# Optimization experiments

Hardware: AMD Instinct MI355X
Metric: run time of the kernel (lower is better)

Reference implementation:

```python
import jax, jax.numpy as jnp
import numpy as np

L, B, E, H = 512, 32, 1024, 16
NEG = -1e9  # finite stand-in for masked_fill(-inf); avoids NaNs if a row were fully masked


def setup_inputs() -> dict:
    key = jax.random.key(0)
    ks = jax.random.split(key, 6)
    s_in = (2.0 / (3 * E + E)) ** 0.5   # xavier-ish scale for in_proj
    s_out = (2.0 / (E + E)) ** 0.5
    return {
        "query": jax.random.normal(ks[0], (L, B, E), jnp.float32),
        "key": jax.random.normal(ks[1], (L, B, E), jnp.float32),
        "value": jax.random.normal(ks[2], (L, B, E), jnp.float32),
        "attn_mask": jax.random.randint(ks[3], (B, L, L), 0, 2).astype(jnp.bool_),
        "in_proj_weight": jax.random.normal(ks[4], (3 * E, E), jnp.float32) * s_in,
        "in_proj_bias": jnp.zeros((3 * E,), jnp.float32),
        "out_proj_weight": jax.random.normal(ks[5], (E, E), jnp.float32) * s_out,
        "out_proj_bias": jnp.zeros((E,), jnp.float32),
        "num_heads": H,
    }


def reference(query, key, value, attn_mask, in_proj_weight, in_proj_bias,
              out_proj_weight, out_proj_bias, num_heads):
    Lq, Bz, Em = query.shape
    hd = Em // num_heads
    Wq, Wk, Wv = jnp.split(in_proj_weight, 3, axis=0)
    bq, bk, bv = jnp.split(in_proj_bias, 3, axis=0)
    # in-projection: x @ W^T + b  (torch F.linear convention)
    q = query @ Wq.T + bq
    k = key @ Wk.T + bk
    v = value @ Wv.T + bv
    # [L, B, E] -> [B*H, L, hd], batch-major (b*H + h) per torch view semantics
    def split_heads(x):
        return x.reshape(x.shape[0], Bz * num_heads, hd).transpose(1, 0, 2)
    q, k, v = split_heads(q), split_heads(k), split_heads(v)
    q = q / jnp.sqrt(jnp.asarray(hd, q.dtype))
    # scores: [B*H, Lq, Lk]
    attn = jnp.einsum('bqd,bkd->bqk', q, k)
    # mask broadcast to heads: [B, L, L] -> [B*H, L, L] with index b*H + h
    mask_mh = jnp.repeat(attn_mask, num_heads, axis=0)
    # original: scatter zeros where masked, then masked_fill(-inf) inside
    # multi_head_positional_attention; net effect = mask -> -inf before softmax
    attn = jnp.where(mask_mh, NEG, attn)
    p = jax.nn.softmax(attn, axis=-1)
    out = jnp.einsum('bqk,bkd->bqd', p, v)        # [B*H, Lq, hd]
    out = out.transpose(1, 0, 2).reshape(Lq, Bz, Em)
    out = out @ out_proj_weight.T + out_proj_bias  # [L, B, E]
    return out
```

## Files before the change

kernel.cpp:

```cpp
#include <hip/hip_runtime.h>
#include <hip/hip_bf16.h>
#include <stdint.h>

#define LSEQ 512
#define BATCH 32
#define EMB 1024
#define NHEAD 16
#define HDIM 64
#define TOK (LSEQ*BATCH)
#define BHTOT (BATCH*NHEAD)

typedef __attribute__((ext_vector_type(8))) short short8;
typedef __attribute__((ext_vector_type(4))) short short4v;
typedef __attribute__((ext_vector_type(4))) float f32x4;

__device__ __forceinline__ short f2bf(float f) {
  __hip_bfloat16 h = __float2bfloat16(f);
  union { __hip_bfloat16 h; short s; } u; u.h = h;
  return u.s;
}

#if defined(__has_builtin)
#if __has_builtin(__builtin_amdgcn_global_load_lds)
#define HAVE_GLL 1
#endif
#endif

__device__ __forceinline__ void gload_lds16(const void* g, void* l) {
#ifdef HAVE_GLL
  __builtin_amdgcn_global_load_lds((const __attribute__((address_space(1))) void*)g,
                                   (__attribute__((address_space(3))) void*)l, 16, 0, 0);
#else
  *(short8*)l = *(const short8*)g;
#endif
}

#define WAIT_VM8  do { asm volatile("s_waitcnt vmcnt(8)" ::: "memory"); __builtin_amdgcn_sched_barrier(0); } while (0)
#define WAIT_VM4  do { asm volatile("s_waitcnt vmcnt(4)" ::: "memory"); __builtin_amdgcn_sched_barrier(0); } while (0)
#define WAIT_VM0  do { asm volatile("s_waitcnt vmcnt(0)" ::: "memory"); __builtin_amdgcn_sched_barrier(0); } while (0)
#define WAIT_LGKM0 do { asm volatile("s_waitcnt lgkmcnt(0)" ::: "memory"); __builtin_amdgcn_sched_barrier(0); } while (0)
#define BAR() __builtin_amdgcn_s_barrier()

__global__ void castx_kernel(const float* __restrict__ xq, const float* __restrict__ xk,
                             const float* __restrict__ xv, short* __restrict__ xb)
{
  const int stride = 4096 * 256;
  int base = blockIdx.x * 256 + threadIdx.x;
  #pragma unroll
  for (int it = 0; it < 12; ++it) {
    int i = base + it * stride;
    const float* src = (i < 4194304) ? xq : (i < 8388608) ? xk : xv;
    int j = i & 4194303;
    f32x4 v = ((const f32x4*)src)[j];
    short4v o;
    o[0] = f2bf(v[0]); o[1] = f2bf(v[1]); o[2] = f2bf(v[2]); o[3] = f2bf(v[3]);
    ((short4v*)xb)[i] = o;
  }
}

__global__ void cast_weights(const float* __restrict__ W, const float* __restrict__ Wo,
                             const float* __restrict__ bias,
                             short* __restrict__ Wb, short* __restrict__ Wob,
                             float* __restrict__ biasp)
{
  int i = blockIdx.x * 256 + threadIdx.x;
  if (i < 786432) {
    f32x4 v = ((const f32x4*)W)[i];
    int row = i >> 8;
    float s = (row < 1024) ? 0.125f : 1.0f;
    short4v o;
    o[0] = f2bf(v[0]*s); o[1] = f2bf(v[1]*s); o[2] = f2bf(v[2]*s); o[3] = f2bf(v[3]*s);
    ((short4v*)Wb)[i] = o;
  } else {
    int j = i - 786432;
    f32x4 v = ((const f32x4*)Wo)[j];
    short4v o;
    o[0] = f2bf(v[0]); o[1] = f2bf(v[1]); o[2] = f2bf(v[2]); o[3] = f2bf(v[3]);
    ((short4v*)Wob)[j] = o;
  }
  if (i < 768) {
    f32x4 v = ((const f32x4*)bias)[i];
    float s = (i < 256) ? 0.125f : 1.0f;
    f32x4 o = {v[0]*s, v[1]*s, v[2]*s, v[3]*s};
    ((f32x4*)biasp)[i] = o;
  }
}

__global__ void maskbits_kernel(const int* __restrict__ mask, uint32_t* __restrict__ mb)
{
  int w = (blockIdx.x * 256 + threadIdx.x) >> 6;
  int lane = threadIdx.x & 63;
  const int* src = mask + ((size_t)w << 9);
  uint32_t* dst = mb + w * 16;
  #pragma unroll
  for (int c = 0; c < 8; ++c) {
    int v = src[c * 64 + lane];
    unsigned long long m = __ballot(v != 0);
    if (lane == 0) dst[c*2]     = (uint32_t)m;
    if (lane == 1) dst[c*2 + 1] = (uint32_t)(m >> 32);
  }
}


#define FRAG_READ(AsX, BsX)                                           \
    short8 af[4], bfr[4];                                             \
    _Pragma("unroll")                                                 \
    for (int mi = 0; mi < 4; ++mi) {                                  \
      int row = wm + mi * 16 + l15;                                   \
      int cs = l4 ^ ((row >> 1) & 3);                                 \
      af[mi] = *(const short8*)&AsX[row * 32 + cs * 8];               \
    }                                                                 \
    _Pragma("unroll")                                                 \
    for (int ni = 0; ni < 4; ++ni) {                                  \
      int row = wn + ni * 16 + l15;                                   \
      int cs = l4 ^ ((row >> 1) & 3);                                 \
      bfr[ni] = *(const short8*)&BsX[row * 32 + cs * 8];              \
    }

#define DO_MFMA()                                                     \
    _Pragma("unroll")                                                 \
    for (int mi = 0; mi < 4; ++mi)                                    \
      _Pragma("unroll")                                               \
      for (int ni = 0; ni < 4; ++ni)                                  \
        acc[mi][ni] = __builtin_amdgcn_mfma_f32_16x16x32_bf16(af[mi], bfr[ni], acc[mi][ni], 0, 0, 0)

#define ISSUE(AsX, BsX, koff)                                         \
    _Pragma("unroll")                                                 \
    for (int jj = 0; jj < 2; ++jj) {                                  \
      gload_lds16(aSrc[jj] + (koff), &AsX[sDst[jj]]);                 \
      gload_lds16(bSrc[jj] + (koff), &BsX[sDst[jj]]);                 \
    }

#define GSTEP_I(AsX, BsX, WAITM, koff)                                \
  { WAITM; BAR();                                                     \
    FRAG_READ(AsX, BsX);                                              \
    WAIT_LGKM0; BAR();                                                \
    ISSUE(AsX, BsX, koff);                                            \
    DO_MFMA(); }

#define GSTEP_N(AsX, BsX, WAITM)                                      \
  { WAITM; BAR();                                                     \
    FRAG_READ(AsX, BsX);                                              \
    WAIT_LGKM0; BAR();                                                \
    DO_MFMA(); }

#define STAGE_COORDS(Abase, Bbase)                                    \
  const short* aSrc[2]; const short* bSrc[2]; int sDst[2];            \
  _Pragma("unroll")                                                   \
  for (int jj = 0; jj < 2; ++jj) {                                    \
    int ch = tid + jj * 256;                                          \
    int row = ch >> 2, cl = ch & 3;                                   \
    int cs = cl ^ ((row >> 1) & 3);                                   \
    aSrc[jj] = (Abase) + (size_t)(m0 + row) * 1024 + cs * 8;          \
    bSrc[jj] = (Bbase) + (size_t)(n0 + row) * 1024 + cs * 8;          \
    sDst[jj] = ch * 8;                                                \
  }

#define PIPE_BODY()                                                   \
        \
  ISSUE(As0, Bs0, 0); ISSUE(As1, Bs1, 32); ISSUE(As2, Bs2, 64);       \
                \
  for (int i = 0; i < 9; ++i) {                                       \
    const int s = 3 * i;                                              \
    GSTEP_I(As0, Bs0, WAIT_VM8, (s + 3) * 32);                        \
    GSTEP_I(As1, Bs1, WAIT_VM8, (s + 4) * 32);                        \
    GSTEP_I(As2, Bs2, WAIT_VM8, (s + 5) * 32);                        \
  }                                                                   \
           \
  GSTEP_I(As0, Bs0, WAIT_VM8, 30 * 32);                               \
  GSTEP_I(As1, Bs1, WAIT_VM8, 31 * 32);                               \
  GSTEP_N(As2, Bs2, WAIT_VM8);                                        \
  GSTEP_N(As0, Bs0, WAIT_VM4);                                        \
  GSTEP_N(As1, Bs1, WAIT_VM0);

__launch_bounds__(256, 3)
__global__ void proj_gemm(const short* __restrict__ xb, const short* __restrict__ W,
                          const float* __restrict__ biasp,
                          short* __restrict__ qh, short* __restrict__ kh,
                          short* __restrict__ vh)
{
  int z = blockIdx.z;
  const short* A = xb + (size_t)z * TOK * EMB;
  short* C       = (z == 0) ? qh : (z == 1) ? kh : vh;
  const short* B = W + (size_t)z * 1024 * 1024;
  const float* bp = biasp + z * 1024;

  int flat = blockIdx.y * 8 + blockIdx.x;
  int X = flat & 7, s0 = flat >> 3;
  int m0 = (X * 16 + (s0 >> 3)) * 128;
  int n0 = (s0 & 7) * 128;

  __shared__ alignas(16) short As0[128 * 32];
  __shared__ alignas(16) short As1[128 * 32];
  __shared__ alignas(16) short As2[128 * 32];
  __shared__ alignas(16) short Bs0[128 * 32];
  __shared__ alignas(16) short Bs1[128 * 32];
  __shared__ alignas(16) short Bs2[128 * 32];

  const int tid = threadIdx.x, lane = tid & 63;
  const int w = tid >> 6;
  const int wm = (w >> 1) * 64, wn = (w & 1) * 64;
  const int l15 = lane & 15, l4 = lane >> 4;

  STAGE_COORDS(A, B);

  f32x4 acc[4][4];
  #pragma unroll
  for (int mi = 0; mi < 4; ++mi)
    #pragma unroll
    for (int ni = 0; ni < 4; ++ni) acc[mi][ni] = f32x4{0.f, 0.f, 0.f, 0.f};

  PIPE_BODY();

  #pragma unroll
  for (int ni = 0; ni < 4; ++ni) {
    int gcol = n0 + wn + ni * 16 + l15;
    float bv = bp[gcol];
    int h = gcol >> 6, d = gcol & 63;
    #pragma unroll
    for (int mi = 0; mi < 4; ++mi) {
      int growb = m0 + wm + mi * 16 + l4 * 4;
      #pragma unroll
      for (int r = 0; r < 4; ++r) {
        int grow = growb + r;
        int lsq = grow >> 5, bb = grow & 31;
        C[((size_t)((bb * NHEAD + h) * LSEQ + lsq)) * HDIM + d] = f2bf(acc[mi][ni][r] + bv);
      }
    }
  }
}

__launch_bounds__(256, 3)
__global__ void out_gemm(const short* __restrict__ Ab, const short* __restrict__ W,
                         const float* __restrict__ bo, float* __restrict__ out)
{
  int flat = blockIdx.y * 8 + blockIdx.x;
  int X = flat & 7, s0 = flat >> 3;
  int m0 = (X * 16 + (s0 >> 3)) * 128;
  int n0 = (s0 & 7) * 128;

  __shared__ alignas(16) short As0[128 * 32];
  __shared__ alignas(16) short As1[128 * 32];
  __shared__ alignas(16) short As2[128 * 32];
  __shared__ alignas(16) short Bs0[128 * 32];
  __shared__ alignas(16) short Bs1[128 * 32];
  __shared__ alignas(16) short Bs2[128 * 32];

  const int tid = threadIdx.x, lane = tid & 63;
  const int w = tid >> 6;
  const int wm = (w >> 1) * 64, wn = (w & 1) * 64;
  const int l15 = lane & 15, l4 = lane >> 4;

  STAGE_COORDS(Ab, W);

  f32x4 acc[4][4];
  #pragma unroll
  for (int mi = 0; mi < 4; ++mi)
    #pragma unroll
    for (int ni = 0; ni < 4; ++ni) acc[mi][ni] = f32x4{0.f, 0.f, 0.f, 0.f};

  PIPE_BODY();

  #pragma unroll
  for (int ni = 0; ni < 4; ++ni) {
    int gcol = n0 + wn + ni * 16 + l15;
    float bv = bo[gcol];
    #pragma unroll
    for (int mi = 0; mi < 4; ++mi) {
      int growb = m0 + wm + mi * 16 + l4 * 4;
      #pragma unroll
      for (int r = 0; r < 4; ++r)
        out[(size_t)(growb + r) * 1024 + gcol] = acc[mi][ni][r] + bv;
    }
  }
}

__launch_bounds__(256, 2)
__global__ void attn_kernel(const short* __restrict__ qh, const short* __restrict__ kh,
                            const short* __restrict__ vh, const uint32_t* __restrict__ mb,
                            short* __restrict__ ao)
{
  int flat = blockIdx.y * 8 + blockIdx.x;
  int X = flat & 7, s = flat >> 3;
  int bh = X * 64 + (s >> 3);
  int qblk = s & 7;
  int b = bh >> 4, h = bh & 15;
  int q0 = qblk * 64;

  const int tid = threadIdx.x, lane = tid & 63, w = tid >> 6;
  const int l15 = lane & 15, l4 = lane >> 4;

  __shared__ alignas(16) short Ks[64 * 64];
  __shared__ alignas(16) short Vt[64 * 72];
  __shared__ alignas(16) short Ps[4 * 16 * 72];
  __shared__ uint32_t Mw[64 * 2];

  const size_t bhoff = (size_t)bh * (LSEQ * HDIM);

  short8 aq[2];
  {
    int qrow = q0 + w * 16 + l15;
    const short* qp = qh + bhoff + (size_t)qrow * HDIM + l4 * 8;
    aq[0] = *(const short8*)qp;
    aq[1] = *(const short8*)(qp + 32);
  }

  f32x4 oacc[4];
  #pragma unroll
  for (int n = 0; n < 4; ++n) oacc[n] = f32x4{0.f, 0.f, 0.f, 0.f};
  float m_i[4], l_i[4];
  #pragma unroll
  for (int r = 0; r < 4; ++r) { m_i[r] = -1e30f; l_i[r] = 0.f; }

  for (int kt = 0; kt < 8; ++kt) {
    __syncthreads();
    #pragma unroll
    for (int jj = 0; jj < 2; ++jj) {
      int ch = tid + jj * 256;
      int row = ch >> 3, cl = ch & 7;
      int cg = cl ^ (row & 7);
      const short* g = kh + bhoff + (size_t)(kt * 64 + row) * HDIM + cg * 8;
      gload_lds16(g, &Ks[ch * 8]);
    }
    #pragma unroll
    for (int jj = 0; jj < 2; ++jj) {
      int c = tid + jj * 256;
      int kv = c & 63, d0 = (c >> 6) * 8;
      const short* g = vh + bhoff + (size_t)(kt * 64 + kv) * HDIM + d0;
      short8 vv = *(const short8*)g;
      #pragma unroll
      for (int j = 0; j < 8; ++j) Vt[(d0 + j) * 72 + kv] = vv[j];
    }
    if (tid < 128) {
      int qr = tid >> 1, wd = tid & 1;
      Mw[qr * 2 + wd] = mb[((size_t)b * LSEQ + q0 + qr) * 16 + kt * 2 + wd];
    }
    __syncthreads();

    f32x4 sa[4];
    #pragma unroll
    for (int n = 0; n < 4; ++n) sa[n] = f32x4{0.f, 0.f, 0.f, 0.f};
    #pragma unroll
    for (int ss = 0; ss < 2; ++ss) {
      #pragma unroll
      for (int n = 0; n < 4; ++n) {
        int row = n * 16 + l15;
        int cs = (ss * 4 + l4) ^ (row & 7);
        short8 bk = *(const short8*)&Ks[row * 64 + cs * 8];
        sa[n] = __builtin_amdgcn_mfma_f32_16x16x32_bf16(aq[ss], bk, sa[n], 0, 0, 0);
      }
    }

    #pragma unroll
    for (int r = 0; r < 4; ++r) {
      int qr = w * 16 + l4 * 4 + r;
      uint32_t mlo = Mw[qr * 2], mhi = Mw[qr * 2 + 1];
      float sv[4];
      #pragma unroll
      for (int n = 0; n < 4; ++n) {
        int cc = n * 16 + l15;
        uint32_t bit = ((cc < 32 ? (mlo >> cc) : (mhi >> (cc - 32))) & 1u);
        sv[n] = bit ? -1e9f : sa[n][r];
      }
      float rmax = fmaxf(fmaxf(sv[0], sv[1]), fmaxf(sv[2], sv[3]));
      #pragma unroll
      for (int off = 1; off < 16; off <<= 1) rmax = fmaxf(rmax, __shfl_xor(rmax, off, 64));
      float mn = fmaxf(m_i[r], rmax);
      float sc = __expf(m_i[r] - mn);
      float p0 = __expf(sv[0] - mn), p1 = __expf(sv[1] - mn);
      float p2 = __expf(sv[2] - mn), p3 = __expf(sv[3] - mn);
      float rs = p0 + p1 + p2 + p3;
      #pragma unroll
      for (int off = 1; off < 16; off <<= 1) rs += __shfl_xor(rs, off, 64);
      l_i[r] = l_i[r] * sc + rs;
      m_i[r] = mn;
      #pragma unroll
      for (int n = 0; n < 4; ++n) oacc[n][r] *= sc;
      short* pp = &Ps[w * 1152 + (l4 * 4 + r) * 72];
      pp[0 * 16 + l15] = f2bf(p0);
      pp[1 * 16 + l15] = f2bf(p1);
      pp[2 * 16 + l15] = f2bf(p2);
      pp[3 * 16 + l15] = f2bf(p3);
    }

    #pragma unroll
    for (int ss = 0; ss < 2; ++ss) {
      short8 pa = *(const short8*)&Ps[w * 1152 + l15 * 72 + ss * 32 + l4 * 8];
      #pragma unroll
      for (int n = 0; n < 4; ++n) {
        short8 bv = *(const short8*)&Vt[(n * 16 + l15) * 72 + ss * 32 + l4 * 8];
        oacc[n] = __builtin_amdgcn_mfma_f32_16x16x32_bf16(pa, bv, oacc[n], 0, 0, 0);
      }
    }
  }

  #pragma unroll
  for (int r = 0; r < 4; ++r) {
    float inv = 1.0f / l_i[r];
    int qrow = q0 + w * 16 + l4 * 4 + r;
    size_t tbase = ((size_t)qrow * BATCH + b) * EMB + h * HDIM;
    #pragma unroll
    for (int n = 0; n < 4; ++n)
      ao[tbase + n * 16 + l15] = f2bf(oacc[n][r] * inv);
  }
}

extern "C" void kernel_launch(void* const* d_in, const int* in_sizes, int n_in,
                              void* d_out, int out_size, void* d_ws, size_t ws_size,
                              hipStream_t stream) {
  const float* q_in = (const float*)d_in[0];
  const float* k_in = (const float*)d_in[1];
  const float* v_in = (const float*)d_in[2];
  const int*   mask = (const int*)d_in[3];
  const float* Wp   = (const float*)d_in[4];
  const float* bp   = (const float*)d_in[5];
  const float* Wo   = (const float*)d_in[6];
  const float* bo   = (const float*)d_in[7];

  char* ws = (char*)d_ws;
  short* Wb    = (short*)ws;    ws += (size_t)3072 * 1024 * 2;
  short* Wob   = (short*)ws;    ws += (size_t)1024 * 1024 * 2;
  float* biasp = (float*)ws;    ws += (size_t)3072 * 4;
  uint32_t* mb = (uint32_t*)ws; ws += (size_t)BATCH * LSEQ * 16 * 4;
  short* qh    = (short*)ws;    ws += (size_t)TOK * EMB * 2;
  short* kh    = (short*)ws;    ws += (size_t)TOK * EMB * 2;
  short* vh    = (short*)ws;    ws += (size_t)TOK * EMB * 2;
  short* xb    = (short*)ws;    ws += (size_t)3 * TOK * EMB * 2;
  short* ao    = xb;

  castx_kernel<<<4096, 256, 0, stream>>>(q_in, k_in, v_in, xb);
  cast_weights<<<4096, 256, 0, stream>>>(Wp, Wo, bp, Wb, Wob, biasp);
  maskbits_kernel<<<4096, 256, 0, stream>>>(mask, mb);
  proj_gemm<<<dim3(8, 128, 3), 256, 0, stream>>>(xb, Wb, biasp, qh, kh, vh);
  attn_kernel<<<dim3(8, 512), 256, 0, stream>>>(qh, kh, vh, mb, ao);
  out_gemm<<<dim3(8, 128), 256, 0, stream>>>(ao, Wob, bo, (float*)d_out);
}
```

Measured before the change: 372.5 us.

## Fuse prep kernels, split projection launches, double attention query tile per block

Merges the three preprocessing kernels (input cast, weight cast, mask bit packing) into a single launch. The projection GEMM is split into three separate launches instead of one grid with a z dimension. The attention kernel now gives each wave 32 query rows instead of 16, so every K/V tile staged in shared memory is reused across twice as many rows and the grid shrinks to half as many blocks. In exchange it uses more registers and shared memory per block and has fewer blocks to spread across the GPU.

```diff
diff --git a/kernel.cpp b/kernel.cpp
--- a/kernel.cpp
+++ b/kernel.cpp
@@ -41,29 +41,26 @@
 #define WAIT_LGKM0 do { asm volatile("s_waitcnt lgkmcnt(0)" ::: "memory"); __builtin_amdgcn_sched_barrier(0); } while (0)
 #define BAR() __builtin_amdgcn_s_barrier()
 
-__global__ void castx_kernel(const float* __restrict__ xq, const float* __restrict__ xk,
-                             const float* __restrict__ xv, short* __restrict__ xb)
+__global__ void prep_kernel(const float* __restrict__ xq, const float* __restrict__ xk,
+                            const float* __restrict__ xv, short* __restrict__ xb,
+                            const float* __restrict__ W, const float* __restrict__ Wo,
+                            const float* __restrict__ bias,
+                            short* __restrict__ Wb, short* __restrict__ Wob,
+                            float* __restrict__ biasp,
+                            const int* __restrict__ mask, uint32_t* __restrict__ mb)
 {
+  const int i = blockIdx.x * 256 + threadIdx.x;
   const int stride = 4096 * 256;
-  int base = blockIdx.x * 256 + threadIdx.x;
   #pragma unroll
   for (int it = 0; it < 12; ++it) {
-    int i = base + it * stride;
-    const float* src = (i < 4194304) ? xq : (i < 8388608) ? xk : xv;
-    int j = i & 4194303;
+    int idx = i + it * stride;
+    const float* src = (idx < 4194304) ? xq : (idx < 8388608) ? xk : xv;
+    int j = idx & 4194303;
     f32x4 v = ((const f32x4*)src)[j];
     short4v o;
     o[0] = f2bf(v[0]); o[1] = f2bf(v[1]); o[2] = f2bf(v[2]); o[3] = f2bf(v[3]);
-    ((short4v*)xb)[i] = o;
-  }
-}
-
-__global__ void cast_weights(const float* __restrict__ W, const float* __restrict__ Wo,
-                             const float* __restrict__ bias,
-                             short* __restrict__ Wb, short* __restrict__ Wob,
-                             float* __restrict__ biasp)
-{
-  int i = blockIdx.x * 256 + threadIdx.x;
+    ((short4v*)xb)[idx] = o;
+  }
   if (i < 786432) {
     f32x4 v = ((const f32x4*)W)[i];
     int row = i >> 8;
@@ -84,20 +81,18 @@
     f32x4 o = {v[0]*s, v[1]*s, v[2]*s, v[3]*s};
     ((f32x4*)biasp)[i] = o;
   }
-}
-
-__global__ void maskbits_kernel(const int* __restrict__ mask, uint32_t* __restrict__ mb)
-{
-  int w = (blockIdx.x * 256 + threadIdx.x) >> 6;
-  int lane = threadIdx.x & 63;
-  const int* src = mask + ((size_t)w << 9);
-  uint32_t* dst = mb + w * 16;
-  #pragma unroll
-  for (int c = 0; c < 8; ++c) {
-    int v = src[c * 64 + lane];
-    unsigned long long m = __ballot(v != 0);
-    if (lane == 0) dst[c*2]     = (uint32_t)m;
-    if (lane == 1) dst[c*2 + 1] = (uint32_t)(m >> 32);
+  {
+    int w = i >> 6;
+    int lane = threadIdx.x & 63;
+    const int* src = mask + ((size_t)w << 9);
+    uint32_t* dst = mb + w * 16;
+    #pragma unroll
+    for (int c = 0; c < 8; ++c) {
+      int v = src[c * 64 + lane];
+      unsigned long long m = __ballot(v != 0);
+      if (lane == 0) dst[c*2]     = (uint32_t)m;
+      if (lane == 1) dst[c*2 + 1] = (uint32_t)(m >> 32);
+    }
   }
 }
 
@@ -157,16 +152,13 @@
   }
 
 #define PIPE_BODY()                                                   \
-        \
   ISSUE(As0, Bs0, 0); ISSUE(As1, Bs1, 32); ISSUE(As2, Bs2, 64);       \
-                \
   for (int i = 0; i < 9; ++i) {                                       \
     const int s = 3 * i;                                              \
     GSTEP_I(As0, Bs0, WAIT_VM8, (s + 3) * 32);                        \
     GSTEP_I(As1, Bs1, WAIT_VM8, (s + 4) * 32);                        \
     GSTEP_I(As2, Bs2, WAIT_VM8, (s + 5) * 32);                        \
   }                                                                   \
-           \
   GSTEP_I(As0, Bs0, WAIT_VM8, 30 * 32);                               \
   GSTEP_I(As1, Bs1, WAIT_VM8, 31 * 32);                               \
   GSTEP_N(As2, Bs2, WAIT_VM8);                                        \
@@ -174,17 +166,9 @@
   GSTEP_N(As1, Bs1, WAIT_VM0);
 
 __launch_bounds__(256, 3)
-__global__ void proj_gemm(const short* __restrict__ xb, const short* __restrict__ W,
-                          const float* __restrict__ biasp,
-                          short* __restrict__ qh, short* __restrict__ kh,
-                          short* __restrict__ vh)
+__global__ void proj_gemm(const short* __restrict__ A, const short* __restrict__ B,
+                          const float* __restrict__ bp, short* __restrict__ C)
 {
-  int z = blockIdx.z;
-  const short* A = xb + (size_t)z * TOK * EMB;
-  short* C       = (z == 0) ? qh : (z == 1) ? kh : vh;
-  const short* B = W + (size_t)z * 1024 * 1024;
-  const float* bp = biasp + z * 1024;
-
   int flat = blockIdx.y * 8 + blockIdx.x;
   int X = flat & 7, s0 = flat >> 3;
   int m0 = (X * 16 + (s0 >> 3)) * 128;
@@ -282,35 +266,39 @@
 {
   int flat = blockIdx.y * 8 + blockIdx.x;
   int X = flat & 7, s = flat >> 3;
-  int bh = X * 64 + (s >> 3);
-  int qblk = s & 7;
+  int bh = X * 64 + (s >> 2);
+  int qblk = s & 3;
   int b = bh >> 4, h = bh & 15;
-  int q0 = qblk * 64;
+  int q0 = qblk * 128;
 
   const int tid = threadIdx.x, lane = tid & 63, w = tid >> 6;
   const int l15 = lane & 15, l4 = lane >> 4;
 
   __shared__ alignas(16) short Ks[64 * 64];
   __shared__ alignas(16) short Vt[64 * 72];
-  __shared__ alignas(16) short Ps[4 * 16 * 72];
-  __shared__ uint32_t Mw[64 * 2];
+  __shared__ alignas(16) short Ps[4 * 32 * 72];
+  __shared__ uint32_t Mw[128 * 2];
 
   const size_t bhoff = (size_t)bh * (LSEQ * HDIM);
 
-  short8 aq[2];
-  {
-    int qrow = q0 + w * 16 + l15;
+  short8 aq[2][2];
+  #pragma unroll
+  for (int m = 0; m < 2; ++m) {
+    int qrow = q0 + w * 32 + m * 16 + l15;
     const short* qp = qh + bhoff + (size_t)qrow * HDIM + l4 * 8;
-    aq[0] = *(const short8*)qp;
-    aq[1] = *(const short8*)(qp + 32);
-  }
-
-  f32x4 oacc[4];
-  #pragma unroll
-  for (int n = 0; n < 4; ++n) oacc[n] = f32x4{0.f, 0.f, 0.f, 0.f};
-  float m_i[4], l_i[4];
-  #pragma unroll
-  for (int r = 0; r < 4; ++r) { m_i[r] = -1e30f; l_i[r] = 0.f; }
+    aq[m][0] = *(const short8*)qp;
+    aq[m][1] = *(const short8*)(qp + 32);
+  }
+
+  f32x4 oacc[2][4];
+  float m_i[2][4], l_i[2][4];
+  #pragma unroll
+  for (int m = 0; m < 2; ++m) {
+    #pragma unroll
+    for (int n = 0; n < 4; ++n) oacc[m][n] = f32x4{0.f, 0.f, 0.f, 0.f};
+    #pragma unroll
+    for (int r = 0; r < 4; ++r) { m_i[m][r] = -1e30f; l_i[m][r] = 0.f; }
+  }
 
   for (int kt = 0; kt < 8; ++kt) {
     __syncthreads();
@@ -331,15 +319,17 @@
       #pragma unroll
       for (int j = 0; j < 8; ++j) Vt[(d0 + j) * 72 + kv] = vv[j];
     }
-    if (tid < 128) {
+    if (tid < 256) {
       int qr = tid >> 1, wd = tid & 1;
       Mw[qr * 2 + wd] = mb[((size_t)b * LSEQ + q0 + qr) * 16 + kt * 2 + wd];
     }
     __syncthreads();
 
-    f32x4 sa[4];
-    #pragma unroll
-    for (int n = 0; n < 4; ++n) sa[n] = f32x4{0.f, 0.f, 0.f, 0.f};
+    f32x4 sa[2][4];
+    #pragma unroll
+    for (int m = 0; m < 2; ++m)
+      #pragma unroll
+      for (int n = 0; n < 4; ++n) sa[m][n] = f32x4{0.f, 0.f, 0.f, 0.f};
     #pragma unroll
     for (int ss = 0; ss < 2; ++ss) {
       #pragma unroll
@@ -347,61 +337,74 @@
         int row = n * 16 + l15;
         int cs = (ss * 4 + l4) ^ (row & 7);
         short8 bk = *(const short8*)&Ks[row * 64 + cs * 8];
-        sa[n] = __builtin_amdgcn_mfma_f32_16x16x32_bf16(aq[ss], bk, sa[n], 0, 0, 0);
+        #pragma unroll
+        for (int m = 0; m < 2; ++m)
+          sa[m][n] = __builtin_amdgcn_mfma_f32_16x16x32_bf16(aq[m][ss], bk, sa[m][n], 0, 0, 0);
       }
     }
 
     #pragma unroll
-    for (int r = 0; r < 4; ++r) {
-      int qr = w * 16 + l4 * 4 + r;
-      uint32_t mlo = Mw[qr * 2], mhi = Mw[qr * 2 + 1];
-      float sv[4];
-      #pragma unroll
-      for (int n = 0; n < 4; ++n) {
-        int cc = n * 16 + l15;
-        uint32_t bit = ((cc < 32 ? (mlo >> cc) : (mhi >> (cc - 32))) & 1u);
-        sv[n] = bit ? -1e9f : sa[n][r];
+    for (int m = 0; m < 2; ++m) {
+      #pragma unroll
+      for (int r = 0; r < 4; ++r) {
+        int qr = w * 32 + m * 16 + l4 * 4 + r;
+        uint32_t mlo = Mw[qr * 2], mhi = Mw[qr * 2 + 1];
+        float sv[4];
+        #pragma unroll
+        for (int n = 0; n < 4; ++n) {
+          int cc = n * 16 + l15;
+          uint32_t bit = ((cc < 32 ? (mlo >> cc) : (mhi >> (cc - 32))) & 1u);
+          sv[n] = bit ? -1e9f : sa[m][n][r];
+        }
+        float rmax = fmaxf(fmaxf(sv[0], sv[1]), fmaxf(sv[2], sv[3]));
+        #pragma unroll
+        for (int off = 1; off < 16; off <<= 1) rmax = fmaxf(rmax, __shfl_xor(rmax, off, 64));
+        float mn = fmaxf(m_i[m][r], rmax);
+        float sc = __expf(m_i[m][r] - mn);
+        float p0 = __expf(sv[0] - mn), p1 = __expf(sv[1] - mn);
+        float p2 = __expf(sv[2] - mn), p3 = __expf(sv[3] - mn);
+        float rs = p0 + p1 + p2 + p3;
+        #pragma unroll
+        for (int off = 1; off < 16; off <<= 1) rs += __shfl_xor(rs, off, 64);
+        l_i[m][r] = l_i[m][r] * sc + rs;
+        m_i[m][r] = mn;
+        #pragma unroll
+        for (int n = 0; n < 4; ++n) oacc[m][n][r] *= sc;
+        short* pp = &Ps[w * 2304 + (m * 16 + l4 * 4 + r) * 72];
+        pp[0 * 16 + l15] = f2bf(p0);
+        pp[1 * 16 + l15] = f2bf(p1);
+        pp[2 * 16 + l15] = f2bf(p2);
+        pp[3 * 16 + l15] = f2bf(p3);
       }
-      float rmax = fmaxf(fmaxf(sv[0], sv[1]), fmaxf(sv[2], sv[3]));
-      #pragma unroll
-      for (int off = 1; off < 16; off <<= 1) rmax = fmaxf(rmax, __shfl_xor(rmax, off, 64));
-      float mn = fmaxf(m_i[r], rmax);
-      float sc = __expf(m_i[r] - mn);
-      float p0 = __expf(sv[0] - mn), p1 = __expf(sv[1] - mn);
-      float p2 = __expf(sv[2] - mn), p3 = __expf(sv[3] - mn);
-      float rs = p0 + p1 + p2 + p3;
-      #pragma unroll
-      for (int off = 1; off < 16; off <<= 1) rs += __shfl_xor(rs, off, 64);
-      l_i[r] = l_i[r] * sc + rs;
-      m_i[r] = mn;
-      #pragma unroll
-      for (int n = 0; n < 4; ++n) oacc[n][r] *= sc;
-      short* pp = &Ps[w * 1152 + (l4 * 4 + r) * 72];
-      pp[0 * 16 + l15] = f2bf(p0);
-      pp[1 * 16 + l15] = f2bf(p1);
-      pp[2 * 16 + l15] = f2bf(p2);
-      pp[3 * 16 + l15] = f2bf(p3);
     }
 
     #pragma unroll
     for (int ss = 0; ss < 2; ++ss) {
-      short8 pa = *(const short8*)&Ps[w * 1152 + l15 * 72 + ss * 32 + l4 * 8];
+      short8 pa[2];
+      #pragma unroll
+      for (int m = 0; m < 2; ++m)
+        pa[m] = *(const short8*)&Ps[w * 2304 + (m * 16 + l15) * 72 + ss * 32 + l4 * 8];
       #pragma unroll
       for (int n = 0; n < 4; ++n) {
         short8 bv = *(const short8*)&Vt[(n * 16 + l15) * 72 + ss * 32 + l4 * 8];
-        oacc[n] = __builtin_amdgcn_mfma_f32_16x16x32_bf16(pa, bv, oacc[n], 0, 0, 0);
+        #pragma unroll
+        for (int m = 0; m < 2; ++m)
+          oacc[m][n] = __builtin_amdgcn_mfma_f32_16x16x32_bf16(pa[m], bv, oacc[m][n], 0, 0, 0);
       }
     }
   }
 
   #pragma unroll
-  for (int r = 0; r < 4; ++r) {
-    float inv = 1.0f / l_i[r];
-    int qrow = q0 + w * 16 + l4 * 4 + r;
-    size_t tbase = ((size_t)qrow * BATCH + b) * EMB + h * HDIM;
-    #pragma unroll
-    for (int n = 0; n < 4; ++n)
-      ao[tbase + n * 16 + l15] = f2bf(oacc[n][r] * inv);
+  for (int m = 0; m < 2; ++m) {
+    #pragma unroll
+    for (int r = 0; r < 4; ++r) {
+      float inv = 1.0f / l_i[m][r];
+      int qrow = q0 + w * 32 + m * 16 + l4 * 4 + r;
+      size_t tbase = ((size_t)qrow * BATCH + b) * EMB + h * HDIM;
+      #pragma unroll
+      for (int n = 0; n < 4; ++n)
+        ao[tbase + n * 16 + l15] = f2bf(oacc[m][n][r] * inv);
+    }
   }
 }
 
@@ -428,10 +431,10 @@
   short* xb    = (short*)ws;    ws += (size_t)3 * TOK * EMB * 2;
   short* ao    = xb;
 
-  castx_kernel<<<4096, 256, 0, stream>>>(q_in, k_in, v_in, xb);
-  cast_weights<<<4096, 256, 0, stream>>>(Wp, Wo, bp, Wb, Wob, biasp);
-  maskbits_kernel<<<4096, 256, 0, stream>>>(mask, mb);
-  proj_gemm<<<dim3(8, 128, 3), 256, 0, stream>>>(xb, Wb, biasp, qh, kh, vh);
-  attn_kernel<<<dim3(8, 512), 256, 0, stream>>>(qh, kh, vh, mb, ao);
+  prep_kernel<<<4096, 256, 0, stream>>>(q_in, k_in, v_in, xb, Wp, Wo, bp, Wb, Wob, biasp, mask, mb);
+  proj_gemm<<<dim3(8, 128), 256, 0, stream>>>(xb,                       Wb,                biasp,        qh);
+  proj_gemm<<<dim3(8, 128), 256, 0, stream>>>(xb + (size_t)TOK * EMB,   Wb + 1024 * 1024,  biasp + 1024, kh);
+  proj_gemm<<<dim3(8, 128), 256, 0, stream>>>(xb + (size_t)2*TOK * EMB, Wb + 2*1024*1024,  biasp + 2048, vh);
+  attn_kernel<<<dim3(8, 256), 256, 0, stream>>>(qh, kh, vh, mb, ao);
   out_gemm<<<dim3(8, 128), 256, 0, stream>>>(ao, Wob, bo, (float*)d_out);
 }
```

Measured after the change: 372.8 us. No clear change (+0.1%).
